# Performance work log

Measured on AMD Instinct MI355X. Metric: run time of the kernel, lower is better.

## Reference

```python
import jax, jax.numpy as jnp
import numpy as np

N, E = 50000, 1600000
IN_DIM, HID, L, H = 300, 256, 3, 4
HD = HID // H  # 64
EPS = 1e-5


def setup_inputs() -> dict:
    key = jax.random.key(0)
    ks = jax.random.split(key, 24)
    s = 0.02
    inp = {
        'node_feats': jax.random.normal(ks[0], (N, IN_DIM), jnp.float32),
        'role': jax.random.randint(ks[1], (N,), 0, 3),
        'edge_src': jax.random.randint(ks[2], (E,), 0, N),
        'edge_dst': jax.random.randint(ks[3], (E,), 0, N),
        'edge_weights': jax.random.uniform(ks[4], (E,), jnp.float32),
        # input role transforms (question / entity / context)
        'Wq': jax.random.normal(ks[5], (IN_DIM, HID), jnp.float32) * s,
        'bq': jnp.zeros((HID,), jnp.float32),
        'We': jax.random.normal(ks[6], (IN_DIM, HID), jnp.float32) * s,
        'be': jnp.zeros((HID,), jnp.float32),
        'Wc': jax.random.normal(ks[7], (IN_DIM, HID), jnp.float32) * s,
        'bc': jnp.zeros((HID,), jnp.float32),
        # per-head value projections [H, HID, HD] (q/k projections omitted:
        # softmax over a scalar == 1.0, so they never affect output or grads)
        'Wv': jax.random.normal(ks[8], (H, HID, HD), jnp.float32) * s,
        'bv': jnp.zeros((H, HD), jnp.float32),
        # shared 'default' edge-type transform (the torch code always falls
        # through to 'default' because edata['rel'] entries are tensors)
        'Wd': jax.random.normal(ks[9], (HD, HD), jnp.float32) * s,
        'bd': jnp.zeros((HD,), jnp.float32),
        # attention_output
        'Wo': jax.random.normal(ks[10], (HID, HID), jnp.float32) * s,
        'bo': jnp.zeros((HID,), jnp.float32),
        # GRUCell params (torch layout: [3*HID, in], gate order r,z,n)
        'W_ih': jax.random.normal(ks[11], (3 * HID, HID), jnp.float32) * s,
        'W_hh': jax.random.normal(ks[12], (3 * HID, HID), jnp.float32) * s,
        'b_ih': jnp.zeros((3 * HID,), jnp.float32),
        'b_hh': jnp.zeros((3 * HID,), jnp.float32),
        # per-layer LayerNorm affine params [L, HID]
        'ln_w': jnp.ones((L, HID), jnp.float32),
        'ln_b': jnp.zeros((L, HID), jnp.float32),
    }
    return inp


def _layernorm(x, w, b):
    mu = jnp.mean(x, -1, keepdims=True)
    var = jnp.mean(jnp.square(x - mu), -1, keepdims=True)
    return (x - mu) * jax.lax.rsqrt(var + EPS) * w + b


def _gru_cell(x, hprev, W_ih, W_hh, b_ih, b_hh):
    gi = x @ W_ih.T + b_ih
    gh = hprev @ W_hh.T + b_hh
    i_r, i_z, i_n = jnp.split(gi, 3, axis=-1)
    h_r, h_z, h_n = jnp.split(gh, 3, axis=-1)
    r = jax.nn.sigmoid(i_r + h_r)
    z = jax.nn.sigmoid(i_z + h_z)
    n = jnp.tanh(i_n + r * h_n)
    return (1.0 - z) * n + z * hprev


def reference(node_feats, role, edge_src, edge_dst, edge_weights,
              Wq, bq, We, be, Wc, bc, Wv, bv, Wd, bd, Wo, bo,
              W_ih, W_hh, b_ih, b_hh, ln_w, ln_b):
    n_nodes = node_feats.shape[0]
    # role-dependent input transform: 0=question, 1=evidence/answer, 2=other
    hq = node_feats @ Wq + bq
    he = node_feats @ We + be
    hc = node_feats @ Wc + bc
    r = role[:, None]
    h = jax.nn.relu(jnp.where(r == 0, hq, jnp.where(r == 1, he, hc)))

    path_mem = jax.lax.stop_gradient(h)  # .detach().clone()
    prev_h = h
    num_layers, num_heads = ln_w.shape[0], Wv.shape[0]
    for layer in range(num_layers):
        head_msgs = []
        for hd in range(num_heads):
            # value proj + shared 'default' edge transform (node-level, fused)
            vt = (h @ Wv[hd] + bv[hd]) @ Wd + bd  # [N, HD]
            # scalar softmax == 1.0 -> attn_weight == edge_weight
            msg = vt[edge_src] * edge_weights[:, None]  # [E, HD]
            head_msgs.append(jax.ops.segment_sum(msg, edge_dst,
                                                 num_segments=n_nodes))
        combined = jnp.concatenate(head_msgs, axis=-1)  # [N, HID]
        path_mem = _gru_cell(combined, path_mem, W_ih, W_hh, b_ih, b_hh)
        h = _layernorm(prev_h + combined @ Wo + bo, ln_w[layer], ln_b[layer])
        # dropout: identity in eval mode
        prev_h = h
    return h + path_mem
```

## Files before the change

### kernel.cpp

```cpp
#include <hip/hip_runtime.h>
#include <math.h>

#define NN 50000
#define EE 1600000
#define IND 300
#define KPAD 320
#define NL 3
#define NBLK 785
#define AGG_NB 12500

typedef unsigned short u16;
typedef __attribute__((ext_vector_type(8))) short short8;
typedef __attribute__((ext_vector_type(4))) float floatx4;

__device__ __forceinline__ float b2f(u16 u) {
  union { unsigned i; float f; } v; v.i = ((unsigned)u) << 16; return v.f;
}
__device__ __forceinline__ u16 f2b(float f) {
  union { unsigned i; float f; } v; v.f = f;
  unsigned b = v.i; b += 0x7fffu + ((b >> 16) & 1u);
  return (u16)(b >> 16);
}
__device__ __forceinline__ float sigf(float x) { return 1.0f / (1.0f + __expf(-x)); }

__global__ void count_kernel(const int* __restrict__ dst, int* __restrict__ cnt) {
  int e = blockIdx.x * 256 + threadIdx.x;
  if (e < EE) atomicAdd(&cnt[dst[e]], 1);
}

__global__ __launch_bounds__(256) void scan1_kernel(const int* __restrict__ cnt,
                                                    int* __restrict__ rs,
                                                    int* __restrict__ bsum) {
  __shared__ int ws[4];
  const int t = threadIdx.x, l = t & 63, w = t >> 6;
  const int base = blockIdx.x * 2048 + t * 8;
  int v[8];
  int tot = 0;
  #pragma unroll
  for (int k = 0; k < 8; ++k) {
    int i = base + k;
    v[k] = (i < NN) ? cnt[i] : 0;
    tot += v[k];
  }
  int x = tot;
  #pragma unroll
  for (int off = 1; off < 64; off <<= 1) {
    int y = __shfl_up(x, off);
    if (l >= off) x += y;
  }
  if (l == 63) ws[w] = x;
  __syncthreads();
  int wpre = 0;
  for (int q = 0; q < w; ++q) wpre += ws[q];
  int run = wpre + (x - tot);
  #pragma unroll
  for (int k = 0; k < 8; ++k) {
    int i = base + k;
    if (i < NN) rs[i] = run;
    run += v[k];
  }
  if (t == 255) bsum[blockIdx.x] = wpre + x;
}

__global__ void scan2_kernel(int* __restrict__ bsum, int nb) {
  int l = threadIdx.x;
  int v = (l < nb) ? bsum[l] : 0;
  int x = v;
  #pragma unroll
  for (int off = 1; off < 64; off <<= 1) {
    int y = __shfl_up(x, off);
    if (l >= off) x += y;
  }
  if (l < nb) bsum[l] = x - v;
  if (l == 63) bsum[nb] = x;
}

__global__ void scan3_kernel(const int* __restrict__ bsum, int* __restrict__ rs, int nb) {
  int i = blockIdx.x * 256 + threadIdx.x;
  if (i < NN) rs[i] += bsum[i >> 11];
  if (i == 0) rs[NN] = bsum[nb];
}

__global__ void fill_kernel(const int* __restrict__ dst, const int* __restrict__ rs,
                            int* __restrict__ ncnt, const int* __restrict__ esrc,
                            const float* __restrict__ ew, int2* __restrict__ srcw) {
  int e = blockIdx.x * 256 + threadIdx.x;
  if (e < EE) {
    int d = dst[e];
    int p = atomicAdd(&ncnt[d], 1);
    int2 v;
    v.x = esrc[e];
    v.y = __float_as_int(ew[e]);
    srcw[rs[d] + p] = v;
  }
}

__global__ void role_count(const int* __restrict__ role, int* __restrict__ cnt3) {
  __shared__ int lc[3];
  if (threadIdx.x < 3) lc[threadIdx.x] = 0;
  __syncthreads();
  int i = blockIdx.x * 256 + threadIdx.x;
  if (i < NN) atomicAdd(&lc[role[i]], 1);
  __syncthreads();
  if (threadIdx.x < 3) atomicAdd(&cnt3[threadIdx.x], lc[threadIdx.x]);
}

__global__ void role_plan(const int* __restrict__ cnt3, int* __restrict__ pbase,
                          int* __restrict__ blkrole) {
  __shared__ int pb[4];
  if (threadIdx.x == 0) {
    pb[0] = 0;
    for (int b = 0; b < 3; ++b) pb[b + 1] = pb[b] + (((cnt3[b] + 63) >> 6) << 6);
    for (int b = 0; b < 4; ++b) pbase[b] = pb[b];
  }
  __syncthreads();
  for (int blk = threadIdx.x; blk < NBLK; blk += 256) {
    int m0 = blk * 64;
    int r = -1;
    for (int b = 0; b < 3; ++b)
      if (m0 >= pb[b] && m0 < pb[b + 1]) r = b;
    blkrole[blk] = r;
  }
}

__global__ void role_fill(const int* __restrict__ role, const int* __restrict__ pbase,
                          int* __restrict__ pos3, int* __restrict__ perm) {
  __shared__ int lcnt[3], lbase[3];
  int i = blockIdx.x * 256 + threadIdx.x;
  if (threadIdx.x < 3) lcnt[threadIdx.x] = 0;
  __syncthreads();
  int r = 0, lr = 0;
  bool valid = (i < NN);
  if (valid) {
    r = role[i];
    lr = atomicAdd(&lcnt[r], 1);
  }
  __syncthreads();
  if (threadIdx.x < 3) lbase[threadIdx.x] = atomicAdd(&pos3[threadIdx.x], lcnt[threadIdx.x]);
  __syncthreads();
  if (valid) perm[pbase[r] + lbase[r] + lr] = i;
}

__global__ void xcast_kernel(const float* __restrict__ X, u16* __restrict__ Xb) {
  size_t i = (size_t)blockIdx.x * 256 + threadIdx.x;
  if (i >= (size_t)NN * KPAD) return;
  int r = (int)(i / KPAD), k = (int)(i % KPAD);
  Xb[i] = (k < IND) ? f2b(X[(size_t)r * IND + k]) : (u16)0;
}

__global__ void wt3_kernel(const float* __restrict__ Wq, const float* __restrict__ We,
                           const float* __restrict__ Wc, u16* __restrict__ Wqt,
                           u16* __restrict__ Wet, u16* __restrict__ Wct) {
  int n = blockIdx.x;
  int which = blockIdx.y;
  const float* W = (which == 0) ? Wq : (which == 1) ? We : Wc;
  u16* Wt = (which == 0) ? Wqt : (which == 1) ? Wet : Wct;
  for (int k = threadIdx.x; k < KPAD; k += 256)
    Wt[(size_t)n * KPAD + k] = (k < IND) ? f2b(W[(size_t)k * 256 + n]) : (u16)0;
}

__global__ void wallt_kernel(const float* __restrict__ Wv, const float* __restrict__ Wd,
                             u16* __restrict__ Wallt) {
  int i = blockIdx.x;
  int c = threadIdx.x;
  int hd = c >> 6, j = c & 63;
  const float* wv = &Wv[hd * (256 * 64) + i * 64];
  float s = 0.f;
  #pragma unroll
  for (int m = 0; m < 64; ++m) s = fmaf(wv[m], Wd[m * 64 + j], s);
  Wallt[(size_t)c * 256 + i] = f2b(s);
}

__global__ void ball_kernel(const float* __restrict__ bv, const float* __restrict__ Wd,
                            const float* __restrict__ bd, float* __restrict__ ball) {
  int c = threadIdx.x;
  int hd = c >> 6, j = c & 63;
  float s = bd[j];
  #pragma unroll
  for (int m = 0; m < 64; ++m) s = fmaf(bv[hd * 64 + m], Wd[m * 64 + j], s);
  ball[c] = s;
}

__global__ void wot_kernel(const float* __restrict__ Wo, u16* __restrict__ Wot) {
  int n = blockIdx.x;
  int k = threadIdx.x;
  Wot[(size_t)n * 256 + k] = f2b(Wo[(size_t)k * 256 + n]);
}

__global__ void castbf2_kernel(const float* __restrict__ s0, const float* __restrict__ s1,
                               u16* __restrict__ d0, u16* __restrict__ d1) {
  int i = blockIdx.x * 256 + threadIdx.x;
  const int n = 768 * 256;
  if (i < n) d0[i] = f2b(s0[i]);
  else if (i < 2 * n) d1[i - n] = f2b(s1[i - n]);
}

#define GEMM_PROLOG \
  __shared__ __align__(16) u16 As[64][72]; \
  __shared__ __align__(16) u16 Bs[64][72]; \
  const int t = threadIdx.x; \
  const int lane = t & 63; \
  const int wv_ = t >> 6; \
  const int wr = wv_ >> 1, wc = wv_ & 1; \
  const int l15 = lane & 15, l4 = lane >> 4; \
  const int srow = t >> 2; \
  const int scol = (t & 3) << 4;

#define STAGE_A(AG, ASTRIDE, VALID, ROWIDX, K0) { \
  int4 v0 = {0, 0, 0, 0}, v1 = {0, 0, 0, 0}; \
  if (VALID) { \
    const int4* p_ = (const int4*)&(AG)[(size_t)(ROWIDX) * (ASTRIDE) + (K0) + scol]; \
    v0 = p_[0]; v1 = p_[1]; \
  } \
  *(int4*)&As[srow][scol] = v0; \
  *(int4*)&As[srow][scol + 8] = v1; }

#define STAGE_B(BG, BSTRIDE, ROWIDX, K0) { \
  const int4* p_ = (const int4*)&(BG)[(size_t)(ROWIDX) * (BSTRIDE) + (K0) + scol]; \
  *(int4*)&Bs[srow][scol] = p_[0]; \
  *(int4*)&Bs[srow][scol + 8] = p_[1]; }

#define MFMA_STEP(ACC) { \
  _Pragma("unroll") \
  for (int kc = 0; kc < 2; ++kc) { \
    short8 a0_ = *(const short8*)&As[wr * 32 + 0 + l15][kc * 32 + l4 * 8]; \
    short8 a1_ = *(const short8*)&As[wr * 32 + 16 + l15][kc * 32 + l4 * 8]; \
    short8 b0_ = *(const short8*)&Bs[wc * 32 + 0 + l15][kc * 32 + l4 * 8]; \
    short8 b1_ = *(const short8*)&Bs[wc * 32 + 16 + l15][kc * 32 + l4 * 8]; \
    ACC[0][0] = __builtin_amdgcn_mfma_f32_16x16x32_bf16(a0_, b0_, ACC[0][0], 0, 0, 0); \
    ACC[0][1] = __builtin_amdgcn_mfma_f32_16x16x32_bf16(a0_, b1_, ACC[0][1], 0, 0, 0); \
    ACC[1][0] = __builtin_amdgcn_mfma_f32_16x16x32_bf16(a1_, b0_, ACC[1][0], 0, 0, 0); \
    ACC[1][1] = __builtin_amdgcn_mfma_f32_16x16x32_bf16(a1_, b1_, ACC[1][1], 0, 0, 0); \
  } }

#define GEMM128_PROLOG \
  __shared__ __align__(16) u16 As[128][72]; \
  __shared__ __align__(16) u16 Bs[128][72]; \
  const int t = threadIdx.x; \
  const int lane = t & 63; \
  const int wv_ = t >> 6; \
  const int qr = (wv_ >> 1) * 64, qc = (wv_ & 1) * 64; \
  const int l15 = lane & 15, l4 = lane >> 4; \
  const int srow = t >> 1; \
  const int scol = (t & 1) * 32;

#define STAGE128_A(AG, ASTRIDE, VALID, ROWIDX, K0) { \
  int4 v0 = {0,0,0,0}, v1 = {0,0,0,0}, v2 = {0,0,0,0}, v3 = {0,0,0,0}; \
  if (VALID) { \
    const int4* p_ = (const int4*)&(AG)[(size_t)(ROWIDX) * (ASTRIDE) + (K0) + scol]; \
    v0 = p_[0]; v1 = p_[1]; v2 = p_[2]; v3 = p_[3]; \
  } \
  *(int4*)&As[srow][scol] = v0; *(int4*)&As[srow][scol + 8] = v1; \
  *(int4*)&As[srow][scol + 16] = v2; *(int4*)&As[srow][scol + 24] = v3; }

#define STAGE128_B(BG, BSTRIDE, ROWIDX, K0) { \
  const int4* p_ = (const int4*)&(BG)[(size_t)(ROWIDX) * (BSTRIDE) + (K0) + scol]; \
  *(int4*)&Bs[srow][scol] = p_[0]; *(int4*)&Bs[srow][scol + 8] = p_[1]; \
  *(int4*)&Bs[srow][scol + 16] = p_[2]; *(int4*)&Bs[srow][scol + 24] = p_[3]; }

#define MFMA128_STEP(ACC) { \
  _Pragma("unroll") \
  for (int kc = 0; kc < 2; ++kc) { \
    short8 af_[4], bf_[4]; \
    _Pragma("unroll") \
    for (int m = 0; m < 4; ++m) af_[m] = *(const short8*)&As[qr + m * 16 + l15][kc * 32 + l4 * 8]; \
    _Pragma("unroll") \
    for (int n = 0; n < 4; ++n) bf_[n] = *(const short8*)&Bs[qc + n * 16 + l15][kc * 32 + l4 * 8]; \
    _Pragma("unroll") \
    for (int m = 0; m < 4; ++m) \
      _Pragma("unroll") \
      for (int n = 0; n < 4; ++n) \
        ACC[m][n] = __builtin_amdgcn_mfma_f32_16x16x32_bf16(af_[m], bf_[n], ACC[m][n], 0, 0, 0); \
  } }

__global__ __launch_bounds__(256) void proj_mfma(
    const u16* __restrict__ Xb, const int* __restrict__ perm,
    const int* __restrict__ blkrole,
    const u16* __restrict__ Wqt, const u16* __restrict__ Wet, const u16* __restrict__ Wct,
    const float* __restrict__ bq, const float* __restrict__ be, const float* __restrict__ bc,
    u16* __restrict__ h, u16* __restrict__ pm) {
  const int brole = blkrole[blockIdx.y];
  if (brole < 0) return;
  GEMM_PROLOG
  const int m0 = blockIdx.y * 64;
  const int n0 = blockIdx.x * 64;
  const u16* Bt = (brole == 0) ? Wqt : (brole == 1) ? Wet : Wct;
  const float* bb = (brole == 0) ? bq : (brole == 1) ? be : bc;
  const int prow = perm[m0 + srow];
  floatx4 acc[2][2] = {};
  for (int k0 = 0; k0 < KPAD; k0 += 64) {
    STAGE_A(Xb, KPAD, prow >= 0, prow, k0)
    STAGE_B(Bt, KPAD, n0 + srow, k0)
    __syncthreads();
    MFMA_STEP(acc)
    __syncthreads();
  }
  #pragma unroll
  for (int m = 0; m < 2; ++m)
    #pragma unroll
    for (int reg = 0; reg < 4; ++reg) {
      int gr = m0 + wr * 32 + m * 16 + l4 * 4 + reg;
      int pr = perm[gr];
      if (pr >= 0) {
        #pragma unroll
        for (int n = 0; n < 2; ++n) {
          int c = n0 + wc * 32 + n * 16 + l15;
          float vo = fmaxf(acc[m][n][reg] + bb[c], 0.f);
          u16 ub = f2b(vo);
          h[(size_t)pr * 256 + c] = ub;
          pm[(size_t)pr * 256 + c] = ub;
        }
      }
    }
}

__global__ __launch_bounds__(256) void vgemm_mfma(
    const u16* __restrict__ A, const u16* __restrict__ Bt,
    const float* __restrict__ bias, u16* __restrict__ C) {
  GEMM128_PROLOG
  const int m0 = blockIdx.y * 128;
  const int n0 = blockIdx.x * 128;
  const int ar = m0 + srow;
  floatx4 acc[4][4] = {};
  for (int k0 = 0; k0 < 256; k0 += 64) {
    STAGE128_A(A, 256, ar < NN, ar, k0)
    STAGE128_B(Bt, 256, n0 + srow, k0)
    __syncthreads();
    MFMA128_STEP(acc)
    __syncthreads();
  }
  #pragma unroll
  for (int m = 0; m < 4; ++m)
    #pragma unroll
    for (int reg = 0; reg < 4; ++reg) {
      int gr = m0 + qr + m * 16 + l4 * 4 + reg;
      if (gr < NN) {
        #pragma unroll
        for (int n = 0; n < 4; ++n) {
          int c = n0 + qc + n * 16 + l15;
          C[(size_t)gr * 256 + c] = f2b(acc[m][n][reg] + bias[c]);
        }
      }
    }
}

__global__ __launch_bounds__(256) void agg_kernel(
    const int2* __restrict__ srcw, const int* __restrict__ rs,
    const u16* __restrict__ V, u16* __restrict__ comb) {
  int bid = blockIdx.x;
  int slice = (bid >= AGG_NB) ? 1 : 0;
  int nb = bid - slice * AGG_NB;
  int n = nb * 4 + (threadIdx.x >> 6);
  int l = threadIdx.x & 63;
  if (n >= NN) return;
  int s = rs[n], e = rs[n + 1];
  const size_t coff = (size_t)(slice << 7) + l * 2;
  float a0 = 0.f, a1 = 0.f, c0 = 0.f, c1 = 0.f;
  for (int base = s; base < e; base += 64) {
    int2 p = {0, 0};
    if (base + l < e) p = srcw[base + l];
    int cnt = min(64, e - base);
    int j = 0;
    for (; j + 4 <= cnt; j += 4) {
      int s0 = __shfl(p.x, j + 0), s1 = __shfl(p.x, j + 1);
      int s2 = __shfl(p.x, j + 2), s3 = __shfl(p.x, j + 3);
      float w0 = __int_as_float(__shfl(p.y, j + 0));
      float w1 = __int_as_float(__shfl(p.y, j + 1));
      float w2 = __int_as_float(__shfl(p.y, j + 2));
      float w3 = __int_as_float(__shfl(p.y, j + 3));
      ushort2 v0 = *(const ushort2*)&V[(size_t)s0 * 256 + coff];
      ushort2 v1 = *(const ushort2*)&V[(size_t)s1 * 256 + coff];
      ushort2 v2 = *(const ushort2*)&V[(size_t)s2 * 256 + coff];
      ushort2 v3 = *(const ushort2*)&V[(size_t)s3 * 256 + coff];
      a0 = fmaf(w0, b2f(v0.x), a0); a1 = fmaf(w0, b2f(v0.y), a1);
      c0 = fmaf(w1, b2f(v1.x), c0); c1 = fmaf(w1, b2f(v1.y), c1);
      a0 = fmaf(w2, b2f(v2.x), a0); a1 = fmaf(w2, b2f(v2.y), a1);
      c0 = fmaf(w3, b2f(v3.x), c0); c1 = fmaf(w3, b2f(v3.y), c1);
    }
    for (; j < cnt; ++j) {
      int src = __shfl(p.x, j);
      float w = __int_as_float(__shfl(p.y, j));
      ushort2 v = *(const ushort2*)&V[(size_t)src * 256 + coff];
      a0 = fmaf(w, b2f(v.x), a0); a1 = fmaf(w, b2f(v.y), a1);
    }
  }
  a0 += c0; a1 += c1;
  ushort2 o;
  o.x = f2b(a0); o.y = f2b(a1);
  *(ushort2*)&comb[(size_t)n * 256 + coff] = o;
}

__global__ __launch_bounds__(256) void gru_mfma(
    const u16* __restrict__ comb, const u16* __restrict__ pmc,
    const u16* __restrict__ Wiht, const u16* __restrict__ Whht,
    const float* __restrict__ bih, const float* __restrict__ bhh,
    u16* __restrict__ pmn) {
  __shared__ __align__(16) u16 As[2][64][72];
  __shared__ __align__(16) u16 Bs[6][64][72];
  const int t = threadIdx.x;
  const int lane = t & 63;
  const int wv_ = t >> 6;
  const int wr = wv_ >> 1, wc = wv_ & 1;
  const int l15 = lane & 15, l4 = lane >> 4;
  const int srow = t >> 2;
  const int scol = (t & 3) << 4;
  const int m0 = blockIdx.y * 64;
  const int cb = blockIdx.x;
  const int ar = m0 + srow;
  const bool av = ar < NN;
  floatx4 acc[6][2][2] = {};
  for (int k0 = 0; k0 < 256; k0 += 64) {
    {
      int4 v0 = {0,0,0,0}, v1 = {0,0,0,0}, u0 = {0,0,0,0}, u1 = {0,0,0,0};
      if (av) {
        const int4* pa = (const int4*)&comb[(size_t)ar * 256 + k0 + scol];
        v0 = pa[0]; v1 = pa[1];
        const int4* pb = (const int4*)&pmc[(size_t)ar * 256 + k0 + scol];
        u0 = pb[0]; u1 = pb[1];
      }
      *(int4*)&As[0][srow][scol] = v0; *(int4*)&As[0][srow][scol + 8] = v1;
      *(int4*)&As[1][srow][scol] = u0; *(int4*)&As[1][srow][scol + 8] = u1;
    }
    #pragma unroll
    for (int g = 0; g < 3; ++g) {
      size_t row = (size_t)(g * 256 + cb * 64 + srow);
      const int4* p1 = (const int4*)&Wiht[row * 256 + k0 + scol];
      *(int4*)&Bs[g][srow][scol] = p1[0];
      *(int4*)&Bs[g][srow][scol + 8] = p1[1];
      const int4* p2 = (const int4*)&Whht[row * 256 + k0 + scol];
      *(int4*)&Bs[3 + g][srow][scol] = p2[0];
      *(int4*)&Bs[3 + g][srow][scol + 8] = p2[1];
    }
    __syncthreads();
    #pragma unroll
    for (int kc = 0; kc < 2; ++kc) {
      short8 a0f[2], a1f[2];
      #pragma unroll
      for (int m = 0; m < 2; ++m) {
        a0f[m] = *(const short8*)&As[0][wr * 32 + m * 16 + l15][kc * 32 + l4 * 8];
        a1f[m] = *(const short8*)&As[1][wr * 32 + m * 16 + l15][kc * 32 + l4 * 8];
      }
      #pragma unroll
      for (int g = 0; g < 3; ++g) {
        short8 b0 = *(const short8*)&Bs[g][wc * 32 + 0 + l15][kc * 32 + l4 * 8];
        short8 b1 = *(const short8*)&Bs[g][wc * 32 + 16 + l15][kc * 32 + l4 * 8];
        acc[g][0][0] = __builtin_amdgcn_mfma_f32_16x16x32_bf16(a0f[0], b0, acc[g][0][0], 0, 0, 0);
        acc[g][0][1] = __builtin_amdgcn_mfma_f32_16x16x32_bf16(a0f[0], b1, acc[g][0][1], 0, 0, 0);
        acc[g][1][0] = __builtin_amdgcn_mfma_f32_16x16x32_bf16(a0f[1], b0, acc[g][1][0], 0, 0, 0);
        acc[g][1][1] = __builtin_amdgcn_mfma_f32_16x16x32_bf16(a0f[1], b1, acc[g][1][1], 0, 0, 0);
      }
      #pragma unroll
      for (int g = 3; g < 6; ++g) {
        short8 b0 = *(const short8*)&Bs[g][wc * 32 + 0 + l15][kc * 32 + l4 * 8];
        short8 b1 = *(const short8*)&Bs[g][wc * 32 + 16 + l15][kc * 32 + l4 * 8];
        acc[g][0][0] = __builtin_amdgcn_mfma_f32_16x16x32_bf16(a1f[0], b0, acc[g][0][0], 0, 0, 0);
        acc[g][0][1] = __builtin_amdgcn_mfma_f32_16x16x32_bf16(a1f[0], b1, acc[g][0][1], 0, 0, 0);
        acc[g][1][0] = __builtin_amdgcn_mfma_f32_16x16x32_bf16(a1f[1], b0, acc[g][1][0], 0, 0, 0);
        acc[g][1][1] = __builtin_amdgcn_mfma_f32_16x16x32_bf16(a1f[1], b1, acc[g][1][1], 0, 0, 0);
      }
    }
    __syncthreads();
  }
  #pragma unroll
  for (int m = 0; m < 2; ++m)
    #pragma unroll
    for (int reg = 0; reg < 4; ++reg) {
      int gr = m0 + wr * 32 + m * 16 + l4 * 4 + reg;
      if (gr < NN) {
        #pragma unroll
        for (int n = 0; n < 2; ++n) {
          int c = cb * 64 + wc * 32 + n * 16 + l15;
          float r = sigf(acc[0][m][n][reg] + acc[3][m][n][reg] + bih[c] + bhh[c]);
          float z = sigf(acc[1][m][n][reg] + acc[4][m][n][reg] + bih[256 + c] + bhh[256 + c]);
          float i_n = acc[2][m][n][reg] + bih[512 + c];
          float h_n = acc[5][m][n][reg] + bhh[512 + c];
          float nn2 = tanhf(i_n + r * h_n);
          float po = b2f(pmc[(size_t)gr * 256 + c]);
          pmn[(size_t)gr * 256 + c] = f2b((1.f - z) * nn2 + z * po);
        }
      }
    }
}

__global__ __launch_bounds__(256) void wo_mfma(
    const u16* __restrict__ comb, const u16* __restrict__ Wot,
    const float* __restrict__ bo, const u16* __restrict__ h,
    u16* __restrict__ tmp) {
  GEMM128_PROLOG
  const int m0 = blockIdx.y * 128;
  const int n0 = blockIdx.x * 128;
  const int ar = m0 + srow;
  floatx4 acc[4][4] = {};
  for (int k0 = 0; k0 < 256; k0 += 64) {
    STAGE128_A(comb, 256, ar < NN, ar, k0)
    STAGE128_B(Wot, 256, n0 + srow, k0)
    __syncthreads();
    MFMA128_STEP(acc)
    __syncthreads();
  }
  #pragma unroll
  for (int m = 0; m < 4; ++m)
    #pragma unroll
    for (int reg = 0; reg < 4; ++reg) {
      int gr = m0 + qr + m * 16 + l4 * 4 + reg;
      if (gr < NN) {
        #pragma unroll
        for (int n = 0; n < 4; ++n) {
          int c = n0 + qc + n * 16 + l15;
          float v = acc[m][n][reg] + bo[c] + b2f(h[(size_t)gr * 256 + c]);
          tmp[(size_t)gr * 256 + c] = f2b(v);
        }
      }
    }
}

__global__ __launch_bounds__(256) void ln_kernel(
    const u16* __restrict__ tmp, u16* __restrict__ h,
    const float* __restrict__ lnw, const float* __restrict__ lnb) {
  int n = blockIdx.x * 4 + (threadIdx.x >> 6);
  int l = threadIdx.x & 63;
  if (n >= NN) return;
  ushort4 v = *(const ushort4*)&tmp[(size_t)n * 256 + l * 4];
  float x0 = b2f(v.x), x1 = b2f(v.y), x2 = b2f(v.z), x3 = b2f(v.w);
  float s = x0 + x1 + x2 + x3;
  #pragma unroll
  for (int off = 1; off < 64; off <<= 1) s += __shfl_xor(s, off);
  float mu = s * (1.f / 256.f);
  float d0 = x0 - mu, d1 = x1 - mu, d2 = x2 - mu, d3 = x3 - mu;
  float vs = d0 * d0 + d1 * d1 + d2 * d2 + d3 * d3;
  #pragma unroll
  for (int off = 1; off < 64; off <<= 1) vs += __shfl_xor(vs, off);
  float inv = rsqrtf(vs * (1.f / 256.f) + 1e-5f);
  int c = l * 4;
  ushort4 o;
  o.x = f2b(d0 * inv * lnw[c + 0] + lnb[c + 0]);
  o.y = f2b(d1 * inv * lnw[c + 1] + lnb[c + 1]);
  o.z = f2b(d2 * inv * lnw[c + 2] + lnb[c + 2]);
  o.w = f2b(d3 * inv * lnw[c + 3] + lnb[c + 3]);
  *(ushort4*)&h[(size_t)n * 256 + c] = o;
}

__global__ __launch_bounds__(256) void ln_final_kernel(
    const u16* __restrict__ tmp, const u16* __restrict__ pm,
    const float* __restrict__ lnw, const float* __restrict__ lnb,
    float* __restrict__ out) {
  int n = blockIdx.x * 4 + (threadIdx.x >> 6);
  int l = threadIdx.x & 63;
  if (n >= NN) return;
  ushort4 v = *(const ushort4*)&tmp[(size_t)n * 256 + l * 4];
  float x0 = b2f(v.x), x1 = b2f(v.y), x2 = b2f(v.z), x3 = b2f(v.w);
  float s = x0 + x1 + x2 + x3;
  #pragma unroll
  for (int off = 1; off < 64; off <<= 1) s += __shfl_xor(s, off);
  float mu = s * (1.f / 256.f);
  float d0 = x0 - mu, d1 = x1 - mu, d2 = x2 - mu, d3 = x3 - mu;
  float vs = d0 * d0 + d1 * d1 + d2 * d2 + d3 * d3;
  #pragma unroll
  for (int off = 1; off < 64; off <<= 1) vs += __shfl_xor(vs, off);
  float inv = rsqrtf(vs * (1.f / 256.f) + 1e-5f);
  int c = l * 4;
  ushort4 pv = *(const ushort4*)&pm[(size_t)n * 256 + c];
  float4 o;
  o.x = b2f(f2b(d0 * inv * lnw[c + 0] + lnb[c + 0])) + b2f(pv.x);
  o.y = b2f(f2b(d1 * inv * lnw[c + 1] + lnb[c + 1])) + b2f(pv.y);
  o.z = b2f(f2b(d2 * inv * lnw[c + 2] + lnb[c + 2])) + b2f(pv.z);
  o.w = b2f(f2b(d3 * inv * lnw[c + 3] + lnb[c + 3])) + b2f(pv.w);
  *(float4*)&out[(size_t)n * 256 + c] = o;
}

extern "C" void kernel_launch(void* const* d_in, const int* in_sizes, int n_in,
                              void* d_out, int out_size, void* d_ws, size_t ws_size,
                              hipStream_t stream) {
  const float* node_feats = (const float*)d_in[0];
  const int* role = (const int*)d_in[1];
  const int* esrc = (const int*)d_in[2];
  const int* edst = (const int*)d_in[3];
  const float* ew = (const float*)d_in[4];
  const float* Wq = (const float*)d_in[5];
  const float* bq = (const float*)d_in[6];
  const float* We = (const float*)d_in[7];
  const float* be = (const float*)d_in[8];
  const float* Wc = (const float*)d_in[9];
  const float* bc = (const float*)d_in[10];
  const float* Wv = (const float*)d_in[11];
  const float* bv = (const float*)d_in[12];
  const float* Wd = (const float*)d_in[13];
  const float* bd = (const float*)d_in[14];
  const float* Wo = (const float*)d_in[15];
  const float* bo = (const float*)d_in[16];
  const float* Wih = (const float*)d_in[17];
  const float* Whh = (const float*)d_in[18];
  const float* bih = (const float*)d_in[19];
  const float* bhh = (const float*)d_in[20];
  const float* lnw = (const float*)d_in[21];
  const float* lnb = (const float*)d_in[22];
  float* out = (float*)d_out;

  char* ws = (char*)d_ws;
  size_t off = 0;
  auto take = [&](size_t bytes) {
    char* p = ws + off;
    off = (off + bytes + 511) & ~(size_t)511;
    return p;
  };
  const size_t NC2 = (size_t)NN * 256 * 2;
  u16* Xb = (u16*)take((size_t)NN * KPAD * 2);
  u16* h = (u16*)take(NC2);
  u16* pm0 = (u16*)take(NC2);
  u16* pm1 = (u16*)take(NC2);
  u16* V = (u16*)take(NC2);
  u16* comb = (u16*)take(NC2);
  u16* tmp = (u16*)take(NC2);
  u16* Wqt = (u16*)take((size_t)256 * KPAD * 2);
  u16* Wet = (u16*)take((size_t)256 * KPAD * 2);
  u16* Wct = (u16*)take((size_t)256 * KPAD * 2);
  u16* Wallt = (u16*)take((size_t)256 * 256 * 2);
  u16* Wot = (u16*)take((size_t)256 * 256 * 2);
  u16* Wiht = (u16*)take((size_t)768 * 256 * 2);
  u16* Whht = (u16*)take((size_t)768 * 256 * 2);
  float* ball = (float*)take(256 * 4);
  int* cnt = (int*)take((size_t)NN * 4);
  int* rs = (int*)take((size_t)(NN + 1) * 4);
  int* ncnt = (int*)take((size_t)NN * 4);
  int2* srcw = (int2*)take((size_t)EE * 8);
  int* cnt3 = (int*)take(16);
  int* pos3 = (int*)take(16);
  int* pbase = (int*)take(16);
  int* blkrole = (int*)take((size_t)NBLK * 4);
  int* perm = (int*)take((size_t)NBLK * 64 * 4);
  int* bsum = (int*)take(64 * 4);

  const int NB_SCAN = (NN + 2047) / 2048;

  hipMemsetAsync(cnt, 0, (size_t)NN * 4, stream);
  hipMemsetAsync(ncnt, 0, (size_t)NN * 4, stream);
  hipMemsetAsync(cnt3, 0, 16, stream);
  hipMemsetAsync(pos3, 0, 16, stream);
  hipMemsetAsync(perm, 0xFF, (size_t)NBLK * 64 * 4, stream);

  count_kernel<<<(EE + 255) / 256, 256, 0, stream>>>(edst, cnt);
  scan1_kernel<<<NB_SCAN, 256, 0, stream>>>(cnt, rs, bsum);
  scan2_kernel<<<1, 64, 0, stream>>>(bsum, NB_SCAN);
  scan3_kernel<<<(NN + 255) / 256, 256, 0, stream>>>(bsum, rs, NB_SCAN);
  fill_kernel<<<(EE + 255) / 256, 256, 0, stream>>>(edst, rs, ncnt, esrc, ew, srcw);

  role_count<<<(NN + 255) / 256, 256, 0, stream>>>(role, cnt3);
  role_plan<<<1, 256, 0, stream>>>(cnt3, pbase, blkrole);
  role_fill<<<(NN + 255) / 256, 256, 0, stream>>>(role, pbase, pos3, perm);

  xcast_kernel<<<(int)(((size_t)NN * KPAD + 255) / 256), 256, 0, stream>>>(node_feats, Xb);
  wt3_kernel<<<dim3(256, 3), 256, 0, stream>>>(Wq, We, Wc, Wqt, Wet, Wct);
  wallt_kernel<<<256, 256, 0, stream>>>(Wv, Wd, Wallt);
  ball_kernel<<<1, 256, 0, stream>>>(bv, Wd, bd, ball);
  wot_kernel<<<256, 256, 0, stream>>>(Wo, Wot);
  castbf2_kernel<<<(2 * 768 * 256 + 255) / 256, 256, 0, stream>>>(Wih, Whh, Wiht, Whht);

  proj_mfma<<<dim3(4, NBLK), 256, 0, stream>>>(Xb, perm, blkrole, Wqt, Wet, Wct,
                                               bq, be, bc, h, pm0);

  u16* pmc = pm0;
  u16* pmn = pm1;
  const int MB128 = (NN + 127) / 128;
  const int MB64 = (NN + 63) / 64;
  for (int layer = 0; layer < NL; ++layer) {
    vgemm_mfma<<<dim3(2, MB128), 256, 0, stream>>>(h, Wallt, ball, V);
    agg_kernel<<<2 * AGG_NB, 256, 0, stream>>>(srcw, rs, V, comb);
    gru_mfma<<<dim3(4, MB64), 256, 0, stream>>>(comb, pmc, Wiht, Whht, bih, bhh, pmn);
    wo_mfma<<<dim3(2, MB128), 256, 0, stream>>>(comb, Wot, bo, h, tmp);
    if (layer < NL - 1) {
      ln_kernel<<<(NN + 3) / 4, 256, 0, stream>>>(tmp, h, lnw + layer * 256, lnb + layer * 256);
    } else {
      ln_final_kernel<<<(NN + 3) / 4, 256, 0, stream>>>(tmp, pmn, lnw + layer * 256,
                                                        lnb + layer * 256, out);
    }
    u16* sw = pmc; pmc = pmn; pmn = sw;
  }
}
```

Baseline: 1.032 ms.

## Fuse Wo GEMM with LayerNorm epilogue and shrink GRU K-tile

The Wo projection is rewritten so each block computes a full 64x256 row tile and applies the residual add and LayerNorm in its epilogue. Row statistics are reduced with shuffles plus shared memory, which removes the separate LN kernels and the bf16 tmp round trip. The final layer writes the output plus path memory directly. Separately, the GRU GEMM K-step drops from 64 to 32, which cuts its LDS footprint to raise occupancy but doubles the number of sync iterations. The fused LN computes variance as E[x^2]-mu^2 in fp32 instead of two passes, and h is read and written in place, which is safe only because each block touches its own rows.

```diff
diff --git a/kernel.cpp b/kernel.cpp
--- a/kernel.cpp
+++ b/kernel.cpp
@@ -395,69 +395,60 @@
     const u16* __restrict__ Wiht, const u16* __restrict__ Whht,
     const float* __restrict__ bih, const float* __restrict__ bhh,
     u16* __restrict__ pmn) {
-  __shared__ __align__(16) u16 As[2][64][72];
-  __shared__ __align__(16) u16 Bs[6][64][72];
+  __shared__ __align__(16) u16 As[2][64][40];
+  __shared__ __align__(16) u16 Bs[6][64][40];
   const int t = threadIdx.x;
   const int lane = t & 63;
   const int wv_ = t >> 6;
   const int wr = wv_ >> 1, wc = wv_ & 1;
   const int l15 = lane & 15, l4 = lane >> 4;
   const int srow = t >> 2;
-  const int scol = (t & 3) << 4;
+  const int kq = (t & 3) << 3;
   const int m0 = blockIdx.y * 64;
   const int cb = blockIdx.x;
   const int ar = m0 + srow;
   const bool av = ar < NN;
   floatx4 acc[6][2][2] = {};
-  for (int k0 = 0; k0 < 256; k0 += 64) {
+  for (int k0 = 0; k0 < 256; k0 += 32) {
     {
-      int4 v0 = {0,0,0,0}, v1 = {0,0,0,0}, u0 = {0,0,0,0}, u1 = {0,0,0,0};
+      int4 v0 = {0, 0, 0, 0}, u0 = {0, 0, 0, 0};
       if (av) {
-        const int4* pa = (const int4*)&comb[(size_t)ar * 256 + k0 + scol];
-        v0 = pa[0]; v1 = pa[1];
-        const int4* pb = (const int4*)&pmc[(size_t)ar * 256 + k0 + scol];
-        u0 = pb[0]; u1 = pb[1];
-      }
-      *(int4*)&As[0][srow][scol] = v0; *(int4*)&As[0][srow][scol + 8] = v1;
-      *(int4*)&As[1][srow][scol] = u0; *(int4*)&As[1][srow][scol + 8] = u1;
+        v0 = *(const int4*)&comb[(size_t)ar * 256 + k0 + kq];
+        u0 = *(const int4*)&pmc[(size_t)ar * 256 + k0 + kq];
+      }
+      *(int4*)&As[0][srow][kq] = v0;
+      *(int4*)&As[1][srow][kq] = u0;
     }
     #pragma unroll
     for (int g = 0; g < 3; ++g) {
       size_t row = (size_t)(g * 256 + cb * 64 + srow);
-      const int4* p1 = (const int4*)&Wiht[row * 256 + k0 + scol];
-      *(int4*)&Bs[g][srow][scol] = p1[0];
-      *(int4*)&Bs[g][srow][scol + 8] = p1[1];
-      const int4* p2 = (const int4*)&Whht[row * 256 + k0 + scol];
-      *(int4*)&Bs[3 + g][srow][scol] = p2[0];
-      *(int4*)&Bs[3 + g][srow][scol + 8] = p2[1];
-    }
-    __syncthreads();
-    #pragma unroll
-    for (int kc = 0; kc < 2; ++kc) {
-      short8 a0f[2], a1f[2];
-      #pragma unroll
-      for (int m = 0; m < 2; ++m) {
-        a0f[m] = *(const short8*)&As[0][wr * 32 + m * 16 + l15][kc * 32 + l4 * 8];
-        a1f[m] = *(const short8*)&As[1][wr * 32 + m * 16 + l15][kc * 32 + l4 * 8];
-      }
-      #pragma unroll
-      for (int g = 0; g < 3; ++g) {
-        short8 b0 = *(const short8*)&Bs[g][wc * 32 + 0 + l15][kc * 32 + l4 * 8];
-        short8 b1 = *(const short8*)&Bs[g][wc * 32 + 16 + l15][kc * 32 + l4 * 8];
-        acc[g][0][0] = __builtin_amdgcn_mfma_f32_16x16x32_bf16(a0f[0], b0, acc[g][0][0], 0, 0, 0);
-        acc[g][0][1] = __builtin_amdgcn_mfma_f32_16x16x32_bf16(a0f[0], b1, acc[g][0][1], 0, 0, 0);
-        acc[g][1][0] = __builtin_amdgcn_mfma_f32_16x16x32_bf16(a0f[1], b0, acc[g][1][0], 0, 0, 0);
-        acc[g][1][1] = __builtin_amdgcn_mfma_f32_16x16x32_bf16(a0f[1], b1, acc[g][1][1], 0, 0, 0);
-      }
-      #pragma unroll
-      for (int g = 3; g < 6; ++g) {
-        short8 b0 = *(const short8*)&Bs[g][wc * 32 + 0 + l15][kc * 32 + l4 * 8];
-        short8 b1 = *(const short8*)&Bs[g][wc * 32 + 16 + l15][kc * 32 + l4 * 8];
-        acc[g][0][0] = __builtin_amdgcn_mfma_f32_16x16x32_bf16(a1f[0], b0, acc[g][0][0], 0, 0, 0);
-        acc[g][0][1] = __builtin_amdgcn_mfma_f32_16x16x32_bf16(a1f[0], b1, acc[g][0][1], 0, 0, 0);
-        acc[g][1][0] = __builtin_amdgcn_mfma_f32_16x16x32_bf16(a1f[1], b0, acc[g][1][0], 0, 0, 0);
-        acc[g][1][1] = __builtin_amdgcn_mfma_f32_16x16x32_bf16(a1f[1], b1, acc[g][1][1], 0, 0, 0);
-      }
+      *(int4*)&Bs[g][srow][kq] = *(const int4*)&Wiht[row * 256 + k0 + kq];
+      *(int4*)&Bs[3 + g][srow][kq] = *(const int4*)&Whht[row * 256 + k0 + kq];
+    }
+    __syncthreads();
+    short8 a0f[2], a1f[2];
+    #pragma unroll
+    for (int m = 0; m < 2; ++m) {
+      a0f[m] = *(const short8*)&As[0][wr * 32 + m * 16 + l15][l4 * 8];
+      a1f[m] = *(const short8*)&As[1][wr * 32 + m * 16 + l15][l4 * 8];
+    }
+    #pragma unroll
+    for (int g = 0; g < 3; ++g) {
+      short8 b0 = *(const short8*)&Bs[g][wc * 32 + 0 + l15][l4 * 8];
+      short8 b1 = *(const short8*)&Bs[g][wc * 32 + 16 + l15][l4 * 8];
+      acc[g][0][0] = __builtin_amdgcn_mfma_f32_16x16x32_bf16(a0f[0], b0, acc[g][0][0], 0, 0, 0);
+      acc[g][0][1] = __builtin_amdgcn_mfma_f32_16x16x32_bf16(a0f[0], b1, acc[g][0][1], 0, 0, 0);
+      acc[g][1][0] = __builtin_amdgcn_mfma_f32_16x16x32_bf16(a0f[1], b0, acc[g][1][0], 0, 0, 0);
+      acc[g][1][1] = __builtin_amdgcn_mfma_f32_16x16x32_bf16(a0f[1], b1, acc[g][1][1], 0, 0, 0);
+    }
+    #pragma unroll
+    for (int g = 3; g < 6; ++g) {
+      short8 b0 = *(const short8*)&Bs[g][wc * 32 + 0 + l15][l4 * 8];
+      short8 b1 = *(const short8*)&Bs[g][wc * 32 + 16 + l15][l4 * 8];
+      acc[g][0][0] = __builtin_amdgcn_mfma_f32_16x16x32_bf16(a1f[0], b0, acc[g][0][0], 0, 0, 0);
+      acc[g][0][1] = __builtin_amdgcn_mfma_f32_16x16x32_bf16(a1f[0], b1, acc[g][0][1], 0, 0, 0);
+      acc[g][1][0] = __builtin_amdgcn_mfma_f32_16x16x32_bf16(a1f[1], b0, acc[g][1][0], 0, 0, 0);
+      acc[g][1][1] = __builtin_amdgcn_mfma_f32_16x16x32_bf16(a1f[1], b1, acc[g][1][1], 0, 0, 0);
     }
     __syncthreads();
   }
@@ -482,90 +473,104 @@
     }
 }
 
-__global__ __launch_bounds__(256) void wo_mfma(
+__global__ __launch_bounds__(256) void wo_ln_mfma(
     const u16* __restrict__ comb, const u16* __restrict__ Wot,
-    const float* __restrict__ bo, const u16* __restrict__ h,
-    u16* __restrict__ tmp) {
-  GEMM128_PROLOG
-  const int m0 = blockIdx.y * 128;
-  const int n0 = blockIdx.x * 128;
-  const int ar = m0 + srow;
+    const float* __restrict__ bo, const u16* __restrict__ h_in,
+    const float* __restrict__ lnw, const float* __restrict__ lnb,
+    u16* __restrict__ h_out, const u16* __restrict__ pm,
+    float* __restrict__ out, int last) {
+  __shared__ __align__(16) u16 As[64][72];
+  __shared__ __align__(16) u16 Bs[256][72];
+  __shared__ float2 red[64][4];
+  const int t = threadIdx.x;
+  const int lane = t & 63;
+  const int w = t >> 6;
+  const int l15 = lane & 15, l4 = lane >> 4;
+  const int m0 = blockIdx.x * 64;
+  const int arow = t >> 2;
+  const int ascol = (t & 3) << 4;
   floatx4 acc[4][4] = {};
   for (int k0 = 0; k0 < 256; k0 += 64) {
-    STAGE128_A(comb, 256, ar < NN, ar, k0)
-    STAGE128_B(Wot, 256, n0 + srow, k0)
-    __syncthreads();
-    MFMA128_STEP(acc)
+    {
+      int r = m0 + arow;
+      int4 v0 = {0, 0, 0, 0}, v1 = {0, 0, 0, 0};
+      if (r < NN) {
+        const int4* p = (const int4*)&comb[(size_t)r * 256 + k0 + ascol];
+        v0 = p[0]; v1 = p[1];
+      }
+      *(int4*)&As[arow][ascol] = v0;
+      *(int4*)&As[arow][ascol + 8] = v1;
+    }
+    {
+      const int4* p = (const int4*)&Wot[(size_t)t * 256 + k0];
+      #pragma unroll
+      for (int q = 0; q < 8; ++q) *(int4*)&Bs[t][q * 8] = p[q];
+    }
+    __syncthreads();
+    #pragma unroll
+    for (int kc = 0; kc < 2; ++kc) {
+      short8 af[4], bf[4];
+      #pragma unroll
+      for (int m = 0; m < 4; ++m) af[m] = *(const short8*)&As[m * 16 + l15][kc * 32 + l4 * 8];
+      #pragma unroll
+      for (int n = 0; n < 4; ++n) bf[n] = *(const short8*)&Bs[w * 64 + n * 16 + l15][kc * 32 + l4 * 8];
+      #pragma unroll
+      for (int m = 0; m < 4; ++m)
+        #pragma unroll
+        for (int n = 0; n < 4; ++n)
+          acc[m][n] = __builtin_amdgcn_mfma_f32_16x16x32_bf16(af[m], bf[n], acc[m][n], 0, 0, 0);
+    }
     __syncthreads();
   }
   #pragma unroll
   for (int m = 0; m < 4; ++m)
     #pragma unroll
     for (int reg = 0; reg < 4; ++reg) {
-      int gr = m0 + qr + m * 16 + l4 * 4 + reg;
+      int rloc = m * 16 + l4 * 4 + reg;
+      int gr = m0 + rloc;
+      float s = 0.f, s2 = 0.f;
+      #pragma unroll
+      for (int n = 0; n < 4; ++n) {
+        int c = w * 64 + n * 16 + l15;
+        float hv = (gr < NN) ? b2f(h_in[(size_t)gr * 256 + c]) : 0.f;
+        float v = acc[m][n][reg] + bo[c] + hv;
+        acc[m][n][reg] = v;
+        s += v;
+        s2 = fmaf(v, v, s2);
+      }
+      #pragma unroll
+      for (int off = 1; off < 16; off <<= 1) {
+        s += __shfl_xor(s, off);
+        s2 += __shfl_xor(s2, off);
+      }
+      if (l15 == 0) red[rloc][w] = make_float2(s, s2);
+    }
+  __syncthreads();
+  #pragma unroll
+  for (int m = 0; m < 4; ++m)
+    #pragma unroll
+    for (int reg = 0; reg < 4; ++reg) {
+      int rloc = m * 16 + l4 * 4 + reg;
+      int gr = m0 + rloc;
+      float2 r0 = red[rloc][0], r1 = red[rloc][1], r2 = red[rloc][2], r3 = red[rloc][3];
+      float tot = (r0.x + r1.x) + (r2.x + r3.x);
+      float tot2 = (r0.y + r1.y) + (r2.y + r3.y);
+      float mu = tot * (1.f / 256.f);
+      float var = tot2 * (1.f / 256.f) - mu * mu;
+      float inv = rsqrtf(fmaxf(var, 0.f) + 1e-5f);
       if (gr < NN) {
         #pragma unroll
         for (int n = 0; n < 4; ++n) {
-          int c = n0 + qc + n * 16 + l15;
-          float v = acc[m][n][reg] + bo[c] + b2f(h[(size_t)gr * 256 + c]);
-          tmp[(size_t)gr * 256 + c] = f2b(v);
+          int c = w * 64 + n * 16 + l15;
+          float lnv = (acc[m][n][reg] - mu) * inv * lnw[c] + lnb[c];
+          if (last) {
+            out[(size_t)gr * 256 + c] = b2f(f2b(lnv)) + b2f(pm[(size_t)gr * 256 + c]);
+          } else {
+            h_out[(size_t)gr * 256 + c] = f2b(lnv);
+          }
         }
       }
     }
-}
-
-__global__ __launch_bounds__(256) void ln_kernel(
-    const u16* __restrict__ tmp, u16* __restrict__ h,
-    const float* __restrict__ lnw, const float* __restrict__ lnb) {
-  int n = blockIdx.x * 4 + (threadIdx.x >> 6);
-  int l = threadIdx.x & 63;
-  if (n >= NN) return;
-  ushort4 v = *(const ushort4*)&tmp[(size_t)n * 256 + l * 4];
-  float x0 = b2f(v.x), x1 = b2f(v.y), x2 = b2f(v.z), x3 = b2f(v.w);
-  float s = x0 + x1 + x2 + x3;
-  #pragma unroll
-  for (int off = 1; off < 64; off <<= 1) s += __shfl_xor(s, off);
-  float mu = s * (1.f / 256.f);
-  float d0 = x0 - mu, d1 = x1 - mu, d2 = x2 - mu, d3 = x3 - mu;
-  float vs = d0 * d0 + d1 * d1 + d2 * d2 + d3 * d3;
-  #pragma unroll
-  for (int off = 1; off < 64; off <<= 1) vs += __shfl_xor(vs, off);
-  float inv = rsqrtf(vs * (1.f / 256.f) + 1e-5f);
-  int c = l * 4;
-  ushort4 o;
-  o.x = f2b(d0 * inv * lnw[c + 0] + lnb[c + 0]);
-  o.y = f2b(d1 * inv * lnw[c + 1] + lnb[c + 1]);
-  o.z = f2b(d2 * inv * lnw[c + 2] + lnb[c + 2]);
-  o.w = f2b(d3 * inv * lnw[c + 3] + lnb[c + 3]);
-  *(ushort4*)&h[(size_t)n * 256 + c] = o;
-}
-
-__global__ __launch_bounds__(256) void ln_final_kernel(
-    const u16* __restrict__ tmp, const u16* __restrict__ pm,
-    const float* __restrict__ lnw, const float* __restrict__ lnb,
-    float* __restrict__ out) {
-  int n = blockIdx.x * 4 + (threadIdx.x >> 6);
-  int l = threadIdx.x & 63;
-  if (n >= NN) return;
-  ushort4 v = *(const ushort4*)&tmp[(size_t)n * 256 + l * 4];
-  float x0 = b2f(v.x), x1 = b2f(v.y), x2 = b2f(v.z), x3 = b2f(v.w);
-  float s = x0 + x1 + x2 + x3;
-  #pragma unroll
-  for (int off = 1; off < 64; off <<= 1) s += __shfl_xor(s, off);
-  float mu = s * (1.f / 256.f);
-  float d0 = x0 - mu, d1 = x1 - mu, d2 = x2 - mu, d3 = x3 - mu;
-  float vs = d0 * d0 + d1 * d1 + d2 * d2 + d3 * d3;
-  #pragma unroll
-  for (int off = 1; off < 64; off <<= 1) vs += __shfl_xor(vs, off);
-  float inv = rsqrtf(vs * (1.f / 256.f) + 1e-5f);
-  int c = l * 4;
-  ushort4 pv = *(const ushort4*)&pm[(size_t)n * 256 + c];
-  float4 o;
-  o.x = b2f(f2b(d0 * inv * lnw[c + 0] + lnb[c + 0])) + b2f(pv.x);
-  o.y = b2f(f2b(d1 * inv * lnw[c + 1] + lnb[c + 1])) + b2f(pv.y);
-  o.z = b2f(f2b(d2 * inv * lnw[c + 2] + lnb[c + 2])) + b2f(pv.z);
-  o.w = b2f(f2b(d3 * inv * lnw[c + 3] + lnb[c + 3])) + b2f(pv.w);
-  *(float4*)&out[(size_t)n * 256 + c] = o;
 }
 
 extern "C" void kernel_launch(void* const* d_in, const int* in_sizes, int n_in,
@@ -610,7 +615,6 @@
   u16* pm1 = (u16*)take(NC2);
   u16* V = (u16*)take(NC2);
   u16* comb = (u16*)take(NC2);
-  u16* tmp = (u16*)take(NC2);
   u16* Wqt = (u16*)take((size_t)256 * KPAD * 2);
   u16* Wet = (u16*)take((size_t)256 * KPAD * 2);
   u16* Wct = (u16*)take((size_t)256 * KPAD * 2);
@@ -666,13 +670,9 @@
     vgemm_mfma<<<dim3(2, MB128), 256, 0, stream>>>(h, Wallt, ball, V);
     agg_kernel<<<2 * AGG_NB, 256, 0, stream>>>(srcw, rs, V, comb);
     gru_mfma<<<dim3(4, MB64), 256, 0, stream>>>(comb, pmc, Wiht, Whht, bih, bhh, pmn);
-    wo_mfma<<<dim3(2, MB128), 256, 0, stream>>>(comb, Wot, bo, h, tmp);
-    if (layer < NL - 1) {
-      ln_kernel<<<(NN + 3) / 4, 256, 0, stream>>>(tmp, h, lnw + layer * 256, lnb + layer * 256);
-    } else {
-      ln_final_kernel<<<(NN + 3) / 4, 256, 0, stream>>>(tmp, pmn, lnw + layer * 256,
-                                                        lnb + layer * 256, out);
-    }
+    wo_ln_mfma<<<MB64, 256, 0, stream>>>(comb, Wot, bo, h,
+                                         lnw + layer * 256, lnb + layer * 256,
+                                         h, pmn, out, (layer == NL - 1) ? 1 : 0);
     u16* sw = pmc; pmc = pmn; pmn = sw;
   }
 }
```

New measurement: 1.169 ms. 13.2% more time.

## Store V in 32-column slabs and aggregate with half-wave edge splitting

Applied to the files above, without the earlier changes.

The value-projection GEMM now writes V as eight column slabs of shape [NN,32], so each gathered source row for one slab is a contiguous 64-byte chunk. The aggregation kernel launches eight slices instead of two. Each wavefront handles one node with two half-waves working on alternating edges, and each lane accumulates one column. A final cross-half shuffle reduces the two partial sums. The intent is to improve the locality of the gathers and L2 reuse per slice, at the cost of re-reading the edge lists eight times and issuing narrower 2-byte loads.

```diff
diff --git a/kernel.cpp b/kernel.cpp
--- a/kernel.cpp
+++ b/kernel.cpp
@@ -316,7 +316,7 @@
 
 __global__ __launch_bounds__(256) void vgemm_mfma(
     const u16* __restrict__ A, const u16* __restrict__ Bt,
-    const float* __restrict__ bias, u16* __restrict__ C) {
+    const float* __restrict__ bias, u16* __restrict__ Vs) {
   GEMM128_PROLOG
   const int m0 = blockIdx.y * 128;
   const int n0 = blockIdx.x * 128;
@@ -338,7 +338,8 @@
         #pragma unroll
         for (int n = 0; n < 4; ++n) {
           int c = n0 + qc + n * 16 + l15;
-          C[(size_t)gr * 256 + c] = f2b(acc[m][n][reg] + bias[c]);
+          size_t off = ((size_t)(c >> 5) * NN + gr) * 32 + (c & 31);
+          Vs[off] = f2b(acc[m][n][reg] + bias[c]);
         }
       }
     }
@@ -346,48 +347,45 @@
 
 __global__ __launch_bounds__(256) void agg_kernel(
     const int2* __restrict__ srcw, const int* __restrict__ rs,
-    const u16* __restrict__ V, u16* __restrict__ comb) {
+    const u16* __restrict__ Vs, u16* __restrict__ comb) {
   int bid = blockIdx.x;
-  int slice = (bid >= AGG_NB) ? 1 : 0;
+  int slice = bid / AGG_NB;
   int nb = bid - slice * AGG_NB;
   int n = nb * 4 + (threadIdx.x >> 6);
-  int l = threadIdx.x & 63;
-  if (n >= NN) return;
+  int lane = threadIdx.x & 63;
+  int hh = lane >> 5;
+  int u = lane & 31;
   int s = rs[n], e = rs[n + 1];
-  const size_t coff = (size_t)(slice << 7) + l * 2;
-  float a0 = 0.f, a1 = 0.f, c0 = 0.f, c1 = 0.f;
+  const u16* __restrict__ vbase = Vs + (size_t)slice * NN * 32;
+  float a0 = 0.f, a1 = 0.f, a2 = 0.f, a3 = 0.f;
   for (int base = s; base < e; base += 64) {
     int2 p = {0, 0};
-    if (base + l < e) p = srcw[base + l];
+    if (base + lane < e) p = srcw[base + lane];
     int cnt = min(64, e - base);
-    int j = 0;
-    for (; j + 4 <= cnt; j += 4) {
-      int s0 = __shfl(p.x, j + 0), s1 = __shfl(p.x, j + 1);
-      int s2 = __shfl(p.x, j + 2), s3 = __shfl(p.x, j + 3);
-      float w0 = __int_as_float(__shfl(p.y, j + 0));
-      float w1 = __int_as_float(__shfl(p.y, j + 1));
-      float w2 = __int_as_float(__shfl(p.y, j + 2));
-      float w3 = __int_as_float(__shfl(p.y, j + 3));
-      ushort2 v0 = *(const ushort2*)&V[(size_t)s0 * 256 + coff];
-      ushort2 v1 = *(const ushort2*)&V[(size_t)s1 * 256 + coff];
-      ushort2 v2 = *(const ushort2*)&V[(size_t)s2 * 256 + coff];
-      ushort2 v3 = *(const ushort2*)&V[(size_t)s3 * 256 + coff];
-      a0 = fmaf(w0, b2f(v0.x), a0); a1 = fmaf(w0, b2f(v0.y), a1);
-      c0 = fmaf(w1, b2f(v1.x), c0); c1 = fmaf(w1, b2f(v1.y), c1);
-      a0 = fmaf(w2, b2f(v2.x), a0); a1 = fmaf(w2, b2f(v2.y), a1);
-      c0 = fmaf(w3, b2f(v3.x), c0); c1 = fmaf(w3, b2f(v3.y), c1);
-    }
-    for (; j < cnt; ++j) {
-      int src = __shfl(p.x, j);
-      float w = __int_as_float(__shfl(p.y, j));
-      ushort2 v = *(const ushort2*)&V[(size_t)src * 256 + coff];
-      a0 = fmaf(w, b2f(v.x), a0); a1 = fmaf(w, b2f(v.y), a1);
-    }
-  }
-  a0 += c0; a1 += c1;
-  ushort2 o;
-  o.x = f2b(a0); o.y = f2b(a1);
-  *(ushort2*)&comb[(size_t)n * 256 + coff] = o;
+    for (int k = 0; k < cnt; k += 8) {
+      int j0 = k + hh, j1 = k + 2 + hh, j2 = k + 4 + hh, j3 = k + 6 + hh;
+      int s0 = __shfl(p.x, j0 & 63), s1 = __shfl(p.x, j1 & 63);
+      int s2 = __shfl(p.x, j2 & 63), s3 = __shfl(p.x, j3 & 63);
+      int w0i = __shfl(p.y, j0 & 63), w1i = __shfl(p.y, j1 & 63);
+      int w2i = __shfl(p.y, j2 & 63), w3i = __shfl(p.y, j3 & 63);
+      bool v0 = j0 < cnt, v1 = j1 < cnt, v2 = j2 < cnt, v3 = j3 < cnt;
+      float w0 = v0 ? __int_as_float(w0i) : 0.f;
+      float w1 = v1 ? __int_as_float(w1i) : 0.f;
+      float w2 = v2 ? __int_as_float(w2i) : 0.f;
+      float w3 = v3 ? __int_as_float(w3i) : 0.f;
+      s0 = v0 ? s0 : 0; s1 = v1 ? s1 : 0;
+      s2 = v2 ? s2 : 0; s3 = v3 ? s3 : 0;
+      float f0 = b2f(vbase[(size_t)s0 * 32 + u]);
+      float f1 = b2f(vbase[(size_t)s1 * 32 + u]);
+      float f2 = b2f(vbase[(size_t)s2 * 32 + u]);
+      float f3 = b2f(vbase[(size_t)s3 * 32 + u]);
+      a0 = fmaf(w0, f0, a0); a1 = fmaf(w1, f1, a1);
+      a2 = fmaf(w2, f2, a2); a3 = fmaf(w3, f3, a3);
+    }
+  }
+  float a = (a0 + a1) + (a2 + a3);
+  a += __shfl_xor(a, 32);
+  if (hh == 0) comb[(size_t)n * 256 + slice * 32 + u] = f2b(a);
 }
 
 __global__ __launch_bounds__(256) void gru_mfma(
@@ -608,7 +606,7 @@
   u16* h = (u16*)take(NC2);
   u16* pm0 = (u16*)take(NC2);
   u16* pm1 = (u16*)take(NC2);
-  u16* V = (u16*)take(NC2);
+  u16* Vs = (u16*)take(NC2);
   u16* comb = (u16*)take(NC2);
   u16* tmp = (u16*)take(NC2);
   u16* Wqt = (u16*)take((size_t)256 * KPAD * 2);
@@ -663,8 +661,8 @@
   const int MB128 = (NN + 127) / 128;
   const int MB64 = (NN + 63) / 64;
   for (int layer = 0; layer < NL; ++layer) {
-    vgemm_mfma<<<dim3(2, MB128), 256, 0, stream>>>(h, Wallt, ball, V);
-    agg_kernel<<<2 * AGG_NB, 256, 0, stream>>>(srcw, rs, V, comb);
+    vgemm_mfma<<<dim3(2, MB128), 256, 0, stream>>>(h, Wallt, ball, Vs);
+    agg_kernel<<<8 * AGG_NB, 256, 0, stream>>>(srcw, rs, Vs, comb);
     gru_mfma<<<dim3(4, MB64), 256, 0, stream>>>(comb, pmc, Wiht, Whht, bih, bhh, pmn);
     wo_mfma<<<dim3(2, MB128), 256, 0, stream>>>(comb, Wot, bo, h, tmp);
     if (layer < NL - 1) {
```

After: 1.289 ms. 24.8% more time.
